# Performance work log

Hardware: AMD Instinct MI355X
Metric: run time of the kernel (lower is better)

## Reference

```python
import jax, jax.numpy as jnp
import numpy as np

NUM_HEADS = 8

def setup_inputs() -> dict:
    key = jax.random.key(0)
    ks = jax.random.split(key, 9)
    b, s, d = 2, 2048, 512
    e = d * NUM_HEADS  # 4096
    sc = 0.02
    return {
        "x": jax.random.normal(ks[0], (b, s, d), jnp.float32),
        "Wq": jax.random.normal(ks[1], (e, d), jnp.float32) * sc,
        "bq": jax.random.normal(ks[2], (e,), jnp.float32) * sc,
        "Wk": jax.random.normal(ks[3], (e, d), jnp.float32) * sc,
        "bk": jax.random.normal(ks[4], (e,), jnp.float32) * sc,
        "Wv": jax.random.normal(ks[5], (e, d), jnp.float32) * sc,
        "bv": jax.random.normal(ks[6], (e,), jnp.float32) * sc,
        "Wo": jax.random.normal(ks[7], (d, e), jnp.float32) * sc,
        "bo": jax.random.normal(ks[8], (d,), jnp.float32) * sc,
    }

def reference(x, Wq, bq, Wk, bk, Wv, bv, Wo, bo):
    b, s, d = x.shape
    h = NUM_HEADS
    hd = d  # head_dim == model_dimension in this module
    # QKV projections: [b, s, h*hd]
    q = (x @ Wq.T + bq).reshape(b, s, h, hd)
    k = (x @ Wk.T + bk).reshape(b, s, h, hd)
    v = (x @ Wv.T + bv).reshape(b, s, h, hd)
    # scores: [b, h, s_q, s_k]
    scores = jnp.einsum("bqhd,bkhd->bhqk", q, k) / jnp.sqrt(jnp.float32(hd))
    attn = jax.nn.softmax(scores, axis=-1)
    ctx = jnp.einsum("bhqk,bkhd->bqhd", attn, v).reshape(b, s, h * hd)
    return ctx @ Wo.T + bo
```

## Files before the change

### kernel.cpp

```cpp
#include <hip/hip_runtime.h>
#include <hip/hip_bf16.h>

typedef __hip_bfloat16 bf16t;
typedef short bf16x8 __attribute__((ext_vector_type(8)));
typedef float f32x4 __attribute__((ext_vector_type(4)));

__device__ __forceinline__ unsigned short f2b(float f) {
    unsigned u;
    __builtin_memcpy(&u, &f, 4);
    unsigned r = (u + 0x7fffu + ((u >> 16) & 1u)) >> 16;
    return (unsigned short)r;
}

__device__ __forceinline__ void gload_lds16(const void* g, void* l) {
    __builtin_amdgcn_global_load_lds(
        (const __attribute__((address_space(1))) void*)g,
        (__attribute__((address_space(3))) void*)l,
        16, 0, 0);
}

__global__ __launch_bounds__(512, 2)
void gemm_qkv(const bf16t* __restrict__ Ag, const bf16t* __restrict__ Bg,
              bf16t* __restrict__ Cg, const float* __restrict__ bias,
              bf16t* __restrict__ VtB, long cOffB)
{
    __shared__ __align__(16) char lds8[131072];

    unsigned gx = gridDim.x, gy = gridDim.y;
    unsigned nwg = gx * gy;
    unsigned wg = blockIdx.y * gx + blockIdx.x;
    if ((nwg & 7u) == 0u) wg = (wg & 7u) * (nwg >> 3) + (wg >> 3);
    const unsigned py = wg / gx;
    const unsigned px = wg - py * gx;
    const int brow = py * 256;
    const int bcol = px * 256;

    const size_t ldab = 1024;
    const size_t ldbb = 1024;
    const char* Agb = (const char*)Ag + (size_t)brow * ldab;
    const char* Bgb = (const char*)Bg + (size_t)bcol * ldbb;

    const int t    = threadIdx.x;
    const int lane = t & 63;
    const int wid  = t >> 6;
    const int wm   = wid >> 2;
    const int wn   = wid & 3;
    const int lr   = lane & 15;
    const int lk   = lane >> 4;

    const int srow = t >> 2;
    const int scg  = (t & 3) ^ ((srow >> 1) & 3);
    const size_t aSrc = (size_t)srow * ldab + (size_t)scg * 16;
    const size_t bSrc = (size_t)srow * ldbb + (size_t)scg * 16;
    const int dst0 = t * 16;
    char* ldsA = lds8;
    char* ldsB = lds8 + 65536;

    const int rchunk = lk ^ ((lr >> 1) & 3);
    const int aByte = (wm * 128 + lr) * 64 + rchunk * 16;
    const int bByte = (wn * 64 + lr) * 64 + rchunk * 16;

    f32x4 acc[8][4];
#pragma unroll
    for (int i = 0; i < 8; ++i)
#pragma unroll
        for (int j = 0; j < 4; ++j)
            acc[i][j] = (f32x4){0.f, 0.f, 0.f, 0.f};

    const int nk = 16;

#define STAGE_A(kt, bufi) do {                                              \
        const char* s_ = Agb + (size_t)(kt) * 64 + aSrc;                    \
        char* d_ = ldsA + (bufi) * 16384 + dst0;                            \
        gload_lds16(s_, d_);                                                \
        gload_lds16(s_ + 128 * ldab, d_ + 8192);                            \
    } while (0)
#define STAGE_B(kt, bufi) do {                                              \
        const char* s_ = Bgb + (size_t)(kt) * 64 + bSrc;                    \
        char* d_ = ldsB + (bufi) * 16384 + dst0;                            \
        gload_lds16(s_, d_);                                                \
        gload_lds16(s_ + 128 * ldbb, d_ + 8192);                            \
    } while (0)

    for (int p = 0; p < 3; ++p) { STAGE_A(p, p & 3); STAGE_B(p, p & 3); }
    asm volatile("s_waitcnt vmcnt(8)" ::: "memory");
    __builtin_amdgcn_s_barrier();

    for (int kt = 0; kt < nk; ++kt) {
        const int buf  = kt & 3;
        const int bufS = (kt + 3) & 3;
        const bool st  = (kt + 3) < nk;
        const char* lA = ldsA + buf * 16384;
        const char* lB = ldsB + buf * 16384;

        bf16x8 af[4], bfv[4];
#pragma unroll
        for (int i = 0; i < 4; ++i) af[i]  = *(const bf16x8*)(lA + aByte + i * 1024);
#pragma unroll
        for (int j = 0; j < 4; ++j) bfv[j] = *(const bf16x8*)(lB + bByte + j * 1024);
        if (st) STAGE_A(kt + 3, bufS);
        __builtin_amdgcn_s_barrier();
        asm volatile("s_waitcnt lgkmcnt(0)" ::: "memory");
        __builtin_amdgcn_s_setprio(1);
#pragma unroll
        for (int i = 0; i < 4; ++i)
#pragma unroll
            for (int j = 0; j < 4; ++j)
                acc[i][j] = __builtin_amdgcn_mfma_f32_16x16x32_bf16(af[i], bfv[j], acc[i][j], 0, 0, 0);
        __builtin_amdgcn_s_setprio(0);
        asm volatile("" ::: "memory");
        __builtin_amdgcn_s_barrier();

        bf16x8 af2[4];
#pragma unroll
        for (int i = 0; i < 4; ++i) af2[i] = *(const bf16x8*)(lA + aByte + (i + 4) * 1024);
        if (st) STAGE_B(kt + 3, bufS);
        if (st)                  asm volatile("s_waitcnt vmcnt(8)" ::: "memory");
        else if (kt + 2 < nk)    asm volatile("s_waitcnt vmcnt(4)" ::: "memory");
        else if (kt + 1 < nk)    asm volatile("s_waitcnt vmcnt(0)" ::: "memory");
        __builtin_amdgcn_s_barrier();
        asm volatile("s_waitcnt lgkmcnt(0)" ::: "memory");
        __builtin_amdgcn_s_setprio(1);
#pragma unroll
        for (int i = 0; i < 4; ++i)
#pragma unroll
            for (int j = 0; j < 4; ++j)
                acc[i + 4][j] = __builtin_amdgcn_mfma_f32_16x16x32_bf16(af2[i], bfv[j], acc[i + 4][j], 0, 0, 0);
        __builtin_amdgcn_s_setprio(0);
        asm volatile("" ::: "memory");
        __builtin_amdgcn_s_barrier();
    }
#undef STAGE_A
#undef STAGE_B

    const int sel = bcol >> 12;
    const int colw0 = bcol & 4095;
    if (sel < 2) {
        __syncthreads();
        unsigned short* lC = (unsigned short*)lds8;
#pragma unroll
        for (int i = 0; i < 8; ++i)
#pragma unroll
            for (int j = 0; j < 4; ++j) {
                int col = wn * 64 + j * 16 + lr;
                float badd = bias[bcol + col];
#pragma unroll
                for (int r = 0; r < 4; ++r) {
                    int row = wm * 128 + i * 16 + lk * 4 + r;
                    lC[row * 256 + col] = f2b(acc[i][j][r] + badd);
                }
            }
        __syncthreads();
        unsigned short* C = (unsigned short*)(Cg + (size_t)sel * cOffB);
#pragma unroll
        for (int p = 0; p < 16; ++p) {
            int c  = p * 512 + t;
            int row = c >> 5;
            int cc  = c & 31;
            bf16x8 v = *(const bf16x8*)(lC + (size_t)c * 8);
            *(bf16x8*)(C + (size_t)(brow + row) * 4096 + colw0 + cc * 8) = v;
        }
    } else {
        unsigned short* C = (unsigned short*)VtB;
#pragma unroll
        for (int i = 0; i < 8; ++i)
#pragma unroll
            for (int j = 0; j < 4; ++j) {
                int col = colw0 + wn * 64 + j * 16 + lr;
                int hh = col >> 9, dd = col & 511;
                float badd = bias[8192 + col];
                int row0 = brow + wm * 128 + i * 16 + lk * 4;
                int bb = row0 >> 11, ss0 = row0 & 2047;
                ushort4 pack;
                pack.x = f2b(acc[i][j][0] + badd);
                pack.y = f2b(acc[i][j][1] + badd);
                pack.z = f2b(acc[i][j][2] + badd);
                pack.w = f2b(acc[i][j][3] + badd);
                size_t addr = ((((size_t)(bb * 8 + hh)) * 512 + dd) << 11) + (size_t)ss0;
                *(ushort4*)(C + addr) = pack;
            }
    }
}

__global__ __launch_bounds__(512, 1)
void attn_fused(const bf16t* __restrict__ Qg, const bf16t* __restrict__ Kg,
                const bf16t* __restrict__ Vtg, bf16t* __restrict__ Esc,
                bf16t* __restrict__ Cg, float scale)
{
    __shared__ __align__(16) char lds[131072];

    unsigned bid = blockIdx.x;
    unsigned swz = (bid & 7u) * 32u + (bid >> 3);
    const int z  = swz >> 4, qt = swz & 15;
    const int zb = z >> 3, zh = z & 7;

    const int t    = threadIdx.x;
    const int lane = t & 63;
    const int wid  = t >> 6;
    const int wm   = wid >> 2;
    const int wn   = wid & 3;
    const int lr   = lane & 15;
    const int lk   = lane >> 4;

    const size_t ldq = 8192;
    const char* Agb = (const char*)Qg + ((size_t)(zb * 2048 + qt * 128) * 4096 + (size_t)zh * 512) * 2;
    const char* Bgb = (const char*)Kg + ((size_t)(zb * 2048) * 4096 + (size_t)zh * 512) * 2;
    unsigned short* Eb = (unsigned short*)(Esc + (size_t)swz * 128 * 2048);

    const int srow = t >> 2;
    const int scg  = (t & 3) ^ ((srow >> 1) & 3);
    const size_t aSrc = (size_t)srow * ldq + (size_t)scg * 16;
    const size_t bSrc = (size_t)srow * ldq + (size_t)scg * 16;
    char* ldsA = lds;
    char* ldsB = lds + 32768;
    const int rchunk = lk ^ ((lr >> 1) & 3);
    const int aByte = (wm * 64 + lr) * 64 + rchunk * 16;
    const int bByte = (wn * 64 + lr) * 64 + rchunk * 16;

    f32x4 acc[4][8];
#pragma unroll
    for (int i = 0; i < 4; ++i)
#pragma unroll
        for (int j = 0; j < 8; ++j)
            acc[i][j] = (f32x4){0.f, 0.f, 0.f, 0.f};
    float rs[4][4];
#pragma unroll
    for (int i = 0; i < 4; ++i)
#pragma unroll
        for (int r = 0; r < 4; ++r)
            rs[i][r] = 0.f;

#define STG_AB(g, bufi) do {                                                \
        gload_lds16(Agb + (size_t)((g) & 15) * 64 + aSrc,                   \
                    ldsA + (bufi) * 8192 + t * 16);                         \
        const char* sb_ = Bgb + (size_t)((g) >> 4) * 256 * ldq              \
                          + (size_t)((g) & 15) * 64 + bSrc;                 \
        char* db_ = ldsB + (bufi) * 16384 + t * 16;                         \
        gload_lds16(sb_, db_);                                              \
        gload_lds16(sb_ + 128 * ldq, db_ + 8192);                           \
    } while (0)

    STG_AB(0, 0); STG_AB(1, 1); STG_AB(2, 2);
    asm volatile("s_waitcnt vmcnt(6)" ::: "memory");
    __builtin_amdgcn_s_barrier();

    for (int g = 0; g < 128; ++g) {
        const int buf = g & 3;
        const char* lA = ldsA + buf * 8192;
        const char* lB = ldsB + buf * 16384;

        bf16x8 af[4], bfv[4];
#pragma unroll
        for (int i = 0; i < 4; ++i) af[i]  = *(const bf16x8*)(lA + aByte + i * 1024);
#pragma unroll
        for (int j = 0; j < 4; ++j) bfv[j] = *(const bf16x8*)(lB + bByte + j * 1024);

        if (g + 3 < 128) {
            STG_AB(g + 3, (g + 3) & 3);
            asm volatile("s_waitcnt vmcnt(6)" ::: "memory");
        } else if (g + 2 < 128) {
            asm volatile("s_waitcnt vmcnt(3)" ::: "memory");
        } else if (g + 1 < 128) {
            asm volatile("s_waitcnt vmcnt(0)" ::: "memory");
        }
        __builtin_amdgcn_s_barrier();
        asm volatile("s_waitcnt lgkmcnt(0)" ::: "memory");
        __builtin_amdgcn_s_setprio(1);
#pragma unroll
        for (int i = 0; i < 4; ++i)
#pragma unroll
            for (int j = 0; j < 4; ++j)
                acc[i][j] = __builtin_amdgcn_mfma_f32_16x16x32_bf16(af[i], bfv[j], acc[i][j], 0, 0, 0);
        __builtin_amdgcn_s_setprio(0);
        asm volatile("" ::: "memory");
        __builtin_amdgcn_s_barrier();

        if ((g & 15) == 15) {
            const int nt = g >> 4;
#pragma unroll
            for (int i = 0; i < 4; ++i)
#pragma unroll
                for (int j = 0; j < 4; ++j)
#pragma unroll
                    for (int r = 0; r < 4; ++r)
                        acc[i][j][r] = __expf(acc[i][j][r] * scale);
#pragma unroll
            for (int i = 0; i < 4; ++i)
#pragma unroll
                for (int r = 0; r < 4; ++r)
                    rs[i][r] += acc[i][0][r] + acc[i][1][r] + acc[i][2][r] + acc[i][3][r];

            unsigned short* epi = (unsigned short*)(lds + 98304);
#pragma unroll
            for (int m = 0; m < 2; ++m) {
                if (wm == m) {
#pragma unroll
                    for (int i = 0; i < 4; ++i)
#pragma unroll
                        for (int j = 0; j < 4; ++j) {
                            int col = wn * 64 + j * 16 + lr;
#pragma unroll
                            for (int r = 0; r < 4; ++r)
                                epi[(i * 16 + lk * 4 + r) * 256 + col] = f2b(acc[i][j][r]);
                        }
                }
                asm volatile("s_waitcnt lgkmcnt(0)" ::: "memory");
                __builtin_amdgcn_s_barrier();
#pragma unroll
                for (int p = 0; p < 4; ++p) {
                    int c  = p * 512 + t;
                    int row = c >> 5;
                    int cc  = c & 31;
                    bf16x8 v = *(const bf16x8*)(epi + (size_t)c * 8);
                    *(bf16x8*)(Eb + (size_t)(m * 64 + row) * 2048 + nt * 256 + cc * 8) = v;
                }
                asm volatile("s_waitcnt lgkmcnt(0)" ::: "memory");
                __builtin_amdgcn_s_barrier();
            }
#pragma unroll
            for (int i = 0; i < 4; ++i)
#pragma unroll
                for (int j = 0; j < 4; ++j)
                    acc[i][j] = (f32x4){0.f, 0.f, 0.f, 0.f};
        }
    }
#undef STG_AB

    asm volatile("s_waitcnt vmcnt(0) lgkmcnt(0)" ::: "memory");
    __builtin_amdgcn_s_barrier();

#pragma unroll
    for (int i = 0; i < 4; ++i)
#pragma unroll
        for (int r = 0; r < 4; ++r) {
            float v = rs[i][r];
            v += __shfl_xor(v, 1);
            v += __shfl_xor(v, 2);
            v += __shfl_xor(v, 4);
            v += __shfl_xor(v, 8);
            rs[i][r] = v;
        }
    float* tbl = (float*)(lds + 98304);
    if (lr == 0) {
#pragma unroll
        for (int i = 0; i < 4; ++i)
#pragma unroll
            for (int r = 0; r < 4; ++r)
                tbl[(wm * 64 + i * 16 + lk * 4 + r) * 4 + wn] = rs[i][r];
    }
    asm volatile("s_waitcnt lgkmcnt(0)" ::: "memory");
    __builtin_amdgcn_s_barrier();
    float inv_[4][4];
#pragma unroll
    for (int i = 0; i < 4; ++i)
#pragma unroll
        for (int r = 0; r < 4; ++r) {
            int row = wm * 64 + i * 16 + lk * 4 + r;
            float4 v4 = *(const float4*)(tbl + row * 4);
            inv_[i][r] = 1.0f / (v4.x + v4.y + v4.z + v4.w);
        }
    asm volatile("s_waitcnt lgkmcnt(0)" ::: "memory");
    __builtin_amdgcn_s_barrier();

    const char* A2 = (const char*)Eb;
    const char* B2 = (const char*)Vtg + (size_t)z * 512 * 2048 * 2;
    char* ldsA2 = lds;
    char* ldsB2 = lds + 24576;
    const size_t a2Src = (size_t)srow * 4096 + (size_t)scg * 16;
    const size_t b2Src = (size_t)srow * 4096 + (size_t)scg * 16;
    const int bByte2 = (wn * 128 + lr) * 64 + rchunk * 16;

#pragma unroll
    for (int i = 0; i < 4; ++i)
#pragma unroll
        for (int j = 0; j < 8; ++j)
            acc[i][j] = (f32x4){0.f, 0.f, 0.f, 0.f};

#define STG_PV(kt, bufi) do {                                               \
        gload_lds16(A2 + (size_t)(kt) * 64 + a2Src,                         \
                    ldsA2 + (bufi) * 8192 + t * 16);                        \
        const char* sb_ = B2 + (size_t)(kt) * 64 + b2Src;                   \
        char* db_ = ldsB2 + (bufi) * 32768 + t * 16;                        \
        gload_lds16(sb_,              db_);                                 \
        gload_lds16(sb_ + 128 * 4096, db_ + 8192);                          \
        gload_lds16(sb_ + 256 * 4096, db_ + 16384);                         \
        gload_lds16(sb_ + 384 * 4096, db_ + 24576);                         \
    } while (0)

    STG_PV(0, 0);
    STG_PV(1, 1);
    asm volatile("s_waitcnt vmcnt(5)" ::: "memory");
    __builtin_amdgcn_s_barrier();

    int bufR = 0, bufS = 2;
    for (int kt = 0; kt < 64; ++kt) {
        const char* lA = ldsA2 + bufR * 8192;
        const char* lB = ldsB2 + bufR * 32768;

        bf16x8 af[4], bfv[8];
#pragma unroll
        for (int i = 0; i < 4; ++i) af[i]  = *(const bf16x8*)(lA + aByte + i * 1024);
#pragma unroll
        for (int j = 0; j < 8; ++j) bfv[j] = *(const bf16x8*)(lB + bByte2 + j * 1024);

        if (kt + 2 < 64) {
            STG_PV(kt + 2, bufS);
            asm volatile("s_waitcnt vmcnt(5)" ::: "memory");
        } else if (kt + 1 < 64) {
            asm volatile("s_waitcnt vmcnt(0)" ::: "memory");
        }
        __builtin_amdgcn_s_barrier();
        asm volatile("s_waitcnt lgkmcnt(0)" ::: "memory");
        __builtin_amdgcn_s_setprio(1);
#pragma unroll
        for (int i = 0; i < 4; ++i)
#pragma unroll
            for (int j = 0; j < 8; ++j)
                acc[i][j] = __builtin_amdgcn_mfma_f32_16x16x32_bf16(af[i], bfv[j], acc[i][j], 0, 0, 0);
        __builtin_amdgcn_s_setprio(0);
        asm volatile("" ::: "memory");
        __builtin_amdgcn_s_barrier();

        bufR = (bufR == 2) ? 0 : bufR + 1;
        bufS = (bufS == 2) ? 0 : bufS + 1;
    }
#undef STG_PV

    unsigned short* lC = (unsigned short*)lds;
    unsigned short* C = (unsigned short*)Cg + (size_t)zb * 2048 * 4096 + (size_t)zh * 512;
#pragma unroll
    for (int m = 0; m < 2; ++m) {
        __syncthreads();
        if (wm == m) {
#pragma unroll
            for (int i = 0; i < 4; ++i)
#pragma unroll
                for (int j = 0; j < 8; ++j) {
                    int col = wn * 128 + j * 16 + lr;
#pragma unroll
                    for (int r = 0; r < 4; ++r) {
                        int row = i * 16 + lk * 4 + r;
                        lC[row * 512 + col] = f2b(acc[i][j][r] * inv_[i][r]);
                    }
                }
        }
        __syncthreads();
#pragma unroll
        for (int p = 0; p < 8; ++p) {
            int c  = p * 512 + t;
            int row = c >> 6;
            int cc  = c & 63;
            bf16x8 v = *(const bf16x8*)(lC + (size_t)c * 8);
            *(bf16x8*)(C + (size_t)(qt * 128 + m * 64 + row) * 4096 + cc * 8) = v;
        }
    }
}

__global__ __launch_bounds__(256, 3)
void gemm_of32(const bf16t* __restrict__ Ag, const bf16t* __restrict__ Bg,
               float* __restrict__ Cg, const float* __restrict__ bias,
               int K, int lda, int ldb, int ldc)
{
    __shared__ __align__(16) char lds[49152];

    unsigned gx = gridDim.x, gy = gridDim.y;
    unsigned nwg = gx * gy;
    unsigned wg = blockIdx.y * gx + blockIdx.x;
    if ((nwg & 7u) == 0u) wg = (wg & 7u) * (nwg >> 3) + (wg >> 3);
    const unsigned py = wg / gx;
    const unsigned px = wg - py * gx;
    const int brow = py * 128;
    const int bcol = px * 64;

    const int t    = threadIdx.x;
    const int lane = t & 63;
    const int wid  = t >> 6;
    const int wr   = wid >> 1, wc = wid & 1;
    const int lr   = lane & 15;
    const int lk   = lane >> 4;

    const size_t ldab = (size_t)lda * 2;
    const size_t ldbb = (size_t)ldb * 2;
    const char* Agb = (const char*)Ag + (size_t)brow * ldab;
    const char* Bgb = (const char*)Bg + (size_t)bcol * ldbb;

    const int srow = t >> 2;
    const int scg  = (t & 3) ^ ((srow >> 1) & 3);
    const size_t aSrc = (size_t)srow * ldab + (size_t)scg * 16;
    const size_t bSrc = (size_t)srow * ldbb + (size_t)scg * 16;
    char* ldsA = lds;
    char* ldsB = lds + 32768;

    const int rchunk = lk ^ ((lr >> 1) & 3);
    const int aByte = (wr * 64 + lr) * 64 + rchunk * 16;
    const int bByte = (wc * 32 + lr) * 64 + rchunk * 16;

    f32x4 acc[4][2];
#pragma unroll
    for (int i = 0; i < 4; ++i)
#pragma unroll
        for (int j = 0; j < 2; ++j)
            acc[i][j] = (f32x4){0.f, 0.f, 0.f, 0.f};

    const int nk = K >> 5;

#define STAGE_O(kt, bufi) do {                                              \
        const char* sa_ = Agb + (size_t)(kt) * 64 + aSrc;                   \
        gload_lds16(sa_,             ldsA + (bufi) * 8192 + t * 16);        \
        gload_lds16(sa_ + 64 * ldab, ldsA + (bufi) * 8192 + 4096 + t * 16); \
        gload_lds16(Bgb + (size_t)(kt) * 64 + bSrc,                         \
                    ldsB + (bufi) * 4096 + t * 16);                         \
    } while (0)

    for (int p = 0; p < 3; ++p) STAGE_O(p, p);
    asm volatile("s_waitcnt vmcnt(6)" ::: "memory");
    __builtin_amdgcn_s_barrier();

    for (int kt = 0; kt < nk; ++kt) {
        const int buf  = kt & 3;
        const bool st  = (kt + 3) < nk;
        const char* lA = ldsA + buf * 8192;
        const char* lB = ldsB + buf * 4096;

        bf16x8 af[4], bfv[2];
#pragma unroll
        for (int i = 0; i < 4; ++i) af[i]  = *(const bf16x8*)(lA + aByte + i * 1024);
#pragma unroll
        for (int j = 0; j < 2; ++j) bfv[j] = *(const bf16x8*)(lB + bByte + j * 1024);
        if (st) STAGE_O(kt + 3, (kt + 3) & 3);
        if (st)                  asm volatile("s_waitcnt vmcnt(6)" ::: "memory");
        else if (kt + 2 < nk)    asm volatile("s_waitcnt vmcnt(3)" ::: "memory");
        else if (kt + 1 < nk)    asm volatile("s_waitcnt vmcnt(0)" ::: "memory");
        __builtin_amdgcn_s_barrier();
        asm volatile("s_waitcnt lgkmcnt(0)" ::: "memory");
        __builtin_amdgcn_s_setprio(1);
#pragma unroll
        for (int i = 0; i < 4; ++i)
#pragma unroll
            for (int j = 0; j < 2; ++j)
                acc[i][j] = __builtin_amdgcn_mfma_f32_16x16x32_bf16(af[i], bfv[j], acc[i][j], 0, 0, 0);
        __builtin_amdgcn_s_setprio(0);
        asm volatile("" ::: "memory");
        __builtin_amdgcn_s_barrier();
    }
#undef STAGE_O

    const int orow = brow + wr * 64;
    const int ocol = bcol + wc * 32;
#pragma unroll
    for (int i = 0; i < 4; ++i)
#pragma unroll
        for (int j = 0; j < 2; ++j) {
            int col = ocol + j * 16 + lr;
            float badd = bias[col];
#pragma unroll
            for (int r = 0; r < 4; ++r) {
                int row = orow + i * 16 + lk * 4 + r;
                Cg[(size_t)row * ldc + col] = acc[i][j][r] + badd;
            }
        }
}

__global__ __launch_bounds__(256)
void cvt6(const float* __restrict__ s0, const float* __restrict__ s1,
          const float* __restrict__ s2, const float* __restrict__ s3,
          const float* __restrict__ s4,
          bf16t* __restrict__ d0, bf16t* __restrict__ d1,
          bf16t* __restrict__ d2, bf16t* __restrict__ d3,
          bf16t* __restrict__ d4,
          const float* __restrict__ bq, const float* __restrict__ bk,
          const float* __restrict__ bv, float* __restrict__ bqkv)
{
    int i = blockIdx.x * 256 + threadIdx.x;
    if (blockIdx.y == 5) {
        if (i < 3072) {
            int e = i * 4;
            const float* src = (e < 4096) ? (bq + e) : (e < 8192) ? (bk + e - 4096) : (bv + e - 8192);
            float4 f = *(const float4*)src;
            *(float4*)(bqkv + e) = f;
        }
        return;
    }
    const float* s;
    bf16t* d;
    switch (blockIdx.y) {
        case 0: s = s0; d = d0; break;
        case 1: s = s1; d = d1; break;
        case 2: s = s2; d = d2; break;
        case 3: s = s3; d = d3; break;
        default: s = s4; d = d4; break;
    }
    float4 f = ((const float4*)s)[i];
    ushort4 o;
    o.x = f2b(f.x); o.y = f2b(f.y); o.z = f2b(f.z); o.w = f2b(f.w);
    ((ushort4*)d)[i] = o;
}

extern "C" void kernel_launch(void* const* d_in, const int* in_sizes, int n_in,
                              void* d_out, int out_size, void* d_ws, size_t ws_size,
                              hipStream_t stream)
{
    const float* x  = (const float*)d_in[0];
    const float* Wq = (const float*)d_in[1];
    const float* bq = (const float*)d_in[2];
    const float* Wk = (const float*)d_in[3];
    const float* bk = (const float*)d_in[4];
    const float* Wv = (const float*)d_in[5];
    const float* bv = (const float*)d_in[6];
    const float* Wo = (const float*)d_in[7];
    const float* bo = (const float*)d_in[8];

    const int Sn = 2048, Dn = 512, En = 4096;
    const int Mn = 4096;
    const float scl = 0.044194173824159216f;

    bf16t* base = (bf16t*)d_ws;
    size_t off = 0;
    bf16t* Qb  = base + off; off += (size_t)Mn * En;
    bf16t* Kb  = base + off; off += (size_t)Mn * En;
    bf16t* Vt  = base + off; off += (size_t)Mn * En;
    bf16t* Xb  = base + off; off += (size_t)Mn * Dn;
    bf16t* Wc  = base + off; off += (size_t)3 * En * Dn;
    bf16t* Wob = base + off; off += (size_t)Dn * En;
    float* Pbias = (float*)(base + off); off += 12288;
    bf16t* Sb  = base + off;

    cvt6<<<dim3(2048, 6, 1), 256, 0, stream>>>(
        x, Wq, Wk, Wv, Wo,
        Xb, Wc, Wc + (size_t)En * Dn, Wc + (size_t)2 * En * Dn, Wob,
        bq, bk, bv, Pbias);

    gemm_qkv<<<dim3(3 * En / 256, Mn / 256, 1), 512, 0, stream>>>(
        Xb, Wc, Qb, Pbias, Vt, (long)Mn * En);

    attn_fused<<<256, 512, 0, stream>>>(Qb, Kb, Vt, Sb, Qb, scl);

    gemm_of32<<<dim3(Dn / 64, Mn / 128, 1), 256, 0, stream>>>(
        Qb, Wob, (float*)d_out, bo, En, En, En, Dn);
}
```

Baseline: 293.7 us.

## Fuse P·V into the QK loop, keeping exp scores in LDS

The attention kernel used to write the full 128x2048 exp-score tile to a global scratch buffer and then run a separate P·V GEMM that read it back. Now, after each 256-key block of QK^T, it writes the exp scores as bf16 into a swizzled LDS region and immediately multiplies them by the matching V^T slab into a persistent accumulator. This removes the global round trip for the scores and the scratch buffer, at the cost of 160KB of LDS, more accumulator registers live at once, and extra barriers per key block. There is still no running max, so it relies on unshifted exp as before.

Measured after the change: 471.7 us. +60.6%, slower.

```diff
diff --git a/kernel.cpp b/kernel.cpp
--- a/kernel.cpp
+++ b/kernel.cpp
@@ -183,11 +183,11 @@
 }
 
 __global__ __launch_bounds__(512, 1)
-void attn_fused(const bf16t* __restrict__ Qg, const bf16t* __restrict__ Kg,
-                const bf16t* __restrict__ Vtg, bf16t* __restrict__ Esc,
-                bf16t* __restrict__ Cg, float scale)
+void attn_flash(const bf16t* __restrict__ Qg, const bf16t* __restrict__ Kg,
+                const bf16t* __restrict__ Vtg, bf16t* __restrict__ Cg,
+                float scale)
 {
-    __shared__ __align__(16) char lds[131072];
+    __shared__ __align__(16) char lds[163840];
 
     unsigned bid = blockIdx.x;
     unsigned swz = (bid & 7u) * 32u + (bid >> 3);
@@ -204,25 +204,29 @@
 
     const size_t ldq = 8192;
     const char* Agb = (const char*)Qg + ((size_t)(zb * 2048 + qt * 128) * 4096 + (size_t)zh * 512) * 2;
-    const char* Bgb = (const char*)Kg + ((size_t)(zb * 2048) * 4096 + (size_t)zh * 512) * 2;
-    unsigned short* Eb = (unsigned short*)(Esc + (size_t)swz * 128 * 2048);
+    const char* Kgb = (const char*)Kg + ((size_t)(zb * 2048) * 4096 + (size_t)zh * 512) * 2;
+    const char* Vgb = (const char*)Vtg + (size_t)z * 512 * 2048 * 2;
 
     const int srow = t >> 2;
     const int scg  = (t & 3) ^ ((srow >> 1) & 3);
-    const size_t aSrc = (size_t)srow * ldq + (size_t)scg * 16;
-    const size_t bSrc = (size_t)srow * ldq + (size_t)scg * 16;
-    char* ldsA = lds;
-    char* ldsB = lds + 32768;
+    const size_t qSrc = (size_t)srow * ldq + (size_t)scg * 16;
+    const size_t vSrc = (size_t)srow * 4096 + (size_t)scg * 16;
+    char* ldsQ = lds;
+    char* ldsK = lds + 32768;
+    char* ldsV = lds;
+    char* Elds = lds + 98304;
+
     const int rchunk = lk ^ ((lr >> 1) & 3);
     const int aByte = (wm * 64 + lr) * 64 + rchunk * 16;
     const int bByte = (wn * 64 + lr) * 64 + rchunk * 16;
-
-    f32x4 acc[4][8];
+    const int vByte = (wn * 128 + lr) * 64 + rchunk * 16;
+
+    f32x4 accC[4][8];
 #pragma unroll
     for (int i = 0; i < 4; ++i)
 #pragma unroll
         for (int j = 0; j < 8; ++j)
-            acc[i][j] = (f32x4){0.f, 0.f, 0.f, 0.f};
+            accC[i][j] = (f32x4){0.f, 0.f, 0.f, 0.f};
     float rs[4][4];
 #pragma unroll
     for (int i = 0; i < 4; ++i)
@@ -230,104 +234,130 @@
         for (int r = 0; r < 4; ++r)
             rs[i][r] = 0.f;
 
-#define STG_AB(g, bufi) do {                                                \
-        gload_lds16(Agb + (size_t)((g) & 15) * 64 + aSrc,                   \
-                    ldsA + (bufi) * 8192 + t * 16);                         \
-        const char* sb_ = Bgb + (size_t)((g) >> 4) * 256 * ldq              \
-                          + (size_t)((g) & 15) * 64 + bSrc;                 \
-        char* db_ = ldsB + (bufi) * 16384 + t * 16;                         \
-        gload_lds16(sb_, db_);                                              \
-        gload_lds16(sb_ + 128 * ldq, db_ + 8192);                           \
+#define STG_QK(nt, ks, bufi) do {                                           \
+        gload_lds16(Agb + (size_t)(ks) * 64 + qSrc,                         \
+                    ldsQ + (bufi) * 8192 + t * 16);                         \
+        const char* sk_ = Kgb + (size_t)(nt) * 256 * ldq                    \
+                          + (size_t)(ks) * 64 + qSrc;                       \
+        char* dk_ = ldsK + (bufi) * 16384 + t * 16;                         \
+        gload_lds16(sk_, dk_);                                              \
+        gload_lds16(sk_ + 128 * ldq, dk_ + 8192);                           \
     } while (0)
-
-    STG_AB(0, 0); STG_AB(1, 1); STG_AB(2, 2);
-    asm volatile("s_waitcnt vmcnt(6)" ::: "memory");
-    __builtin_amdgcn_s_barrier();
-
-    for (int g = 0; g < 128; ++g) {
-        const int buf = g & 3;
-        const char* lA = ldsA + buf * 8192;
-        const char* lB = ldsB + buf * 16384;
-
-        bf16x8 af[4], bfv[4];
-#pragma unroll
-        for (int i = 0; i < 4; ++i) af[i]  = *(const bf16x8*)(lA + aByte + i * 1024);
-#pragma unroll
-        for (int j = 0; j < 4; ++j) bfv[j] = *(const bf16x8*)(lB + bByte + j * 1024);
-
-        if (g + 3 < 128) {
-            STG_AB(g + 3, (g + 3) & 3);
-            asm volatile("s_waitcnt vmcnt(6)" ::: "memory");
-        } else if (g + 2 < 128) {
-            asm volatile("s_waitcnt vmcnt(3)" ::: "memory");
-        } else if (g + 1 < 128) {
-            asm volatile("s_waitcnt vmcnt(0)" ::: "memory");
-        }
-        __builtin_amdgcn_s_barrier();
+#define STG_V(nt, c, bufi) do {                                             \
+        const char* sv_ = Vgb + (size_t)(nt) * 512 + (size_t)(c) * 64 + vSrc;\
+        char* dv_ = ldsV + (bufi) * 32768 + t * 16;                         \
+        gload_lds16(sv_,              dv_);                                 \
+        gload_lds16(sv_ + 128 * 4096, dv_ + 8192);                          \
+        gload_lds16(sv_ + 256 * 4096, dv_ + 16384);                         \
+        gload_lds16(sv_ + 384 * 4096, dv_ + 24576);                         \
+    } while (0)
+
+    for (int nt = 0; nt < 8; ++nt) {
+        f32x4 accA[4][4];
+#pragma unroll
+        for (int i = 0; i < 4; ++i)
+#pragma unroll
+            for (int j = 0; j < 4; ++j)
+                accA[i][j] = (f32x4){0.f, 0.f, 0.f, 0.f};
+
+        STG_QK(nt, 0, 0); STG_QK(nt, 1, 1); STG_QK(nt, 2, 2);
+        asm volatile("s_waitcnt vmcnt(6)" ::: "memory");
+        __builtin_amdgcn_s_barrier();
+
+        for (int ks = 0; ks < 16; ++ks) {
+            const int buf = ks & 3;
+            const char* lA = ldsQ + buf * 8192;
+            const char* lB = ldsK + buf * 16384;
+
+            bf16x8 af[4], bfv[4];
+#pragma unroll
+            for (int i = 0; i < 4; ++i) af[i]  = *(const bf16x8*)(lA + aByte + i * 1024);
+#pragma unroll
+            for (int j = 0; j < 4; ++j) bfv[j] = *(const bf16x8*)(lB + bByte + j * 1024);
+
+            if (ks + 3 < 16) {
+                STG_QK(nt, ks + 3, (ks + 3) & 3);
+                asm volatile("s_waitcnt vmcnt(6)" ::: "memory");
+            } else if (ks + 2 < 16) {
+                asm volatile("s_waitcnt vmcnt(3)" ::: "memory");
+            } else if (ks + 1 < 16) {
+                asm volatile("s_waitcnt vmcnt(0)" ::: "memory");
+            }
+            __builtin_amdgcn_s_barrier();
+            asm volatile("s_waitcnt lgkmcnt(0)" ::: "memory");
+            __builtin_amdgcn_s_setprio(1);
+#pragma unroll
+            for (int i = 0; i < 4; ++i)
+#pragma unroll
+                for (int j = 0; j < 4; ++j)
+                    accA[i][j] = __builtin_amdgcn_mfma_f32_16x16x32_bf16(af[i], bfv[j], accA[i][j], 0, 0, 0);
+            __builtin_amdgcn_s_setprio(0);
+            asm volatile("" ::: "memory");
+            __builtin_amdgcn_s_barrier();
+        }
+
+        unsigned short* Ew = (unsigned short*)Elds;
+#pragma unroll
+        for (int i = 0; i < 4; ++i)
+#pragma unroll
+            for (int j = 0; j < 4; ++j) {
+                int col = wn * 64 + j * 16 + lr;
+#pragma unroll
+                for (int r = 0; r < 4; ++r) {
+                    float e = __expf(accA[i][j][r] * scale);
+                    accA[i][j][r] = e;
+                    int row = wm * 64 + i * 16 + lk * 4 + r;
+                    int slot = (col >> 3) ^ (row & 7);
+                    Ew[row * 256 + slot * 8 + (col & 7)] = f2b(e);
+                }
+            }
+#pragma unroll
+        for (int i = 0; i < 4; ++i)
+#pragma unroll
+            for (int r = 0; r < 4; ++r)
+                rs[i][r] += accA[i][0][r] + accA[i][1][r] + accA[i][2][r] + accA[i][3][r];
         asm volatile("s_waitcnt lgkmcnt(0)" ::: "memory");
-        __builtin_amdgcn_s_setprio(1);
-#pragma unroll
-        for (int i = 0; i < 4; ++i)
-#pragma unroll
-            for (int j = 0; j < 4; ++j)
-                acc[i][j] = __builtin_amdgcn_mfma_f32_16x16x32_bf16(af[i], bfv[j], acc[i][j], 0, 0, 0);
-        __builtin_amdgcn_s_setprio(0);
-        asm volatile("" ::: "memory");
-        __builtin_amdgcn_s_barrier();
-
-        if ((g & 15) == 15) {
-            const int nt = g >> 4;
+        __builtin_amdgcn_s_barrier();
+
+        STG_V(nt, 0, 0); STG_V(nt, 1, 1);
+        asm volatile("s_waitcnt vmcnt(4)" ::: "memory");
+        __builtin_amdgcn_s_barrier();
+
+        for (int c = 0; c < 8; ++c) {
+            const int bufv = c % 3;
+            const char* lV = ldsV + bufv * 32768;
+
+            bf16x8 afE[4], bfvV[8];
+#pragma unroll
+            for (int i = 0; i < 4; ++i) {
+                int row = wm * 64 + i * 16 + lr;
+                int slot = (c * 4 + lk) ^ (lr & 7);
+                afE[i] = *(const bf16x8*)(Elds + (size_t)row * 512 + (size_t)slot * 16);
+            }
+#pragma unroll
+            for (int j = 0; j < 8; ++j) bfvV[j] = *(const bf16x8*)(lV + vByte + j * 1024);
+
+            if (c + 2 < 8) {
+                STG_V(nt, c + 2, (c + 2) % 3);
+                asm volatile("s_waitcnt vmcnt(4)" ::: "memory");
+            } else if (c + 1 < 8) {
+                asm volatile("s_waitcnt vmcnt(0)" ::: "memory");
+            }
+            __builtin_amdgcn_s_barrier();
+            asm volatile("s_waitcnt lgkmcnt(0)" ::: "memory");
+            __builtin_amdgcn_s_setprio(1);
 #pragma unroll
             for (int i = 0; i < 4; ++i)
 #pragma unroll
-                for (int j = 0; j < 4; ++j)
-#pragma unroll
-                    for (int r = 0; r < 4; ++r)
-                        acc[i][j][r] = __expf(acc[i][j][r] * scale);
-#pragma unroll
-            for (int i = 0; i < 4; ++i)
-#pragma unroll
-                for (int r = 0; r < 4; ++r)
-                    rs[i][r] += acc[i][0][r] + acc[i][1][r] + acc[i][2][r] + acc[i][3][r];
-
-            unsigned short* epi = (unsigned short*)(lds + 98304);
-#pragma unroll
-            for (int m = 0; m < 2; ++m) {
-                if (wm == m) {
-#pragma unroll
-                    for (int i = 0; i < 4; ++i)
-#pragma unroll
-                        for (int j = 0; j < 4; ++j) {
-                            int col = wn * 64 + j * 16 + lr;
-#pragma unroll
-                            for (int r = 0; r < 4; ++r)
-                                epi[(i * 16 + lk * 4 + r) * 256 + col] = f2b(acc[i][j][r]);
-                        }
-                }
-                asm volatile("s_waitcnt lgkmcnt(0)" ::: "memory");
-                __builtin_amdgcn_s_barrier();
-#pragma unroll
-                for (int p = 0; p < 4; ++p) {
-                    int c  = p * 512 + t;
-                    int row = c >> 5;
-                    int cc  = c & 31;
-                    bf16x8 v = *(const bf16x8*)(epi + (size_t)c * 8);
-                    *(bf16x8*)(Eb + (size_t)(m * 64 + row) * 2048 + nt * 256 + cc * 8) = v;
-                }
-                asm volatile("s_waitcnt lgkmcnt(0)" ::: "memory");
-                __builtin_amdgcn_s_barrier();
-            }
-#pragma unroll
-            for (int i = 0; i < 4; ++i)
-#pragma unroll
-                for (int j = 0; j < 4; ++j)
-                    acc[i][j] = (f32x4){0.f, 0.f, 0.f, 0.f};
-        }
-    }
-#undef STG_AB
-
-    asm volatile("s_waitcnt vmcnt(0) lgkmcnt(0)" ::: "memory");
-    __builtin_amdgcn_s_barrier();
+                for (int j = 0; j < 8; ++j)
+                    accC[i][j] = __builtin_amdgcn_mfma_f32_16x16x32_bf16(afE[i], bfvV[j], accC[i][j], 0, 0, 0);
+            __builtin_amdgcn_s_setprio(0);
+            asm volatile("" ::: "memory");
+            __builtin_amdgcn_s_barrier();
+        }
+    }
+#undef STG_QK
+#undef STG_V
 
 #pragma unroll
     for (int i = 0; i < 4; ++i)
@@ -340,7 +370,8 @@
             v += __shfl_xor(v, 8);
             rs[i][r] = v;
         }
-    float* tbl = (float*)(lds + 98304);
+    __syncthreads();
+    float* tbl = (float*)Elds;
     if (lr == 0) {
 #pragma unroll
         for (int i = 0; i < 4; ++i)
@@ -348,8 +379,7 @@
             for (int r = 0; r < 4; ++r)
                 tbl[(wm * 64 + i * 16 + lk * 4 + r) * 4 + wn] = rs[i][r];
     }
-    asm volatile("s_waitcnt lgkmcnt(0)" ::: "memory");
-    __builtin_amdgcn_s_barrier();
+    __syncthreads();
     float inv_[4][4];
 #pragma unroll
     for (int i = 0; i < 4; ++i)
@@ -359,72 +389,6 @@
             float4 v4 = *(const float4*)(tbl + row * 4);
             inv_[i][r] = 1.0f / (v4.x + v4.y + v4.z + v4.w);
         }
-    asm volatile("s_waitcnt lgkmcnt(0)" ::: "memory");
-    __builtin_amdgcn_s_barrier();
-
-    const char* A2 = (const char*)Eb;
-    const char* B2 = (const char*)Vtg + (size_t)z * 512 * 2048 * 2;
-    char* ldsA2 = lds;
-    char* ldsB2 = lds + 24576;
-    const size_t a2Src = (size_t)srow * 4096 + (size_t)scg * 16;
-    const size_t b2Src = (size_t)srow * 4096 + (size_t)scg * 16;
-    const int bByte2 = (wn * 128 + lr) * 64 + rchunk * 16;
-
-#pragma unroll
-    for (int i = 0; i < 4; ++i)
-#pragma unroll
-        for (int j = 0; j < 8; ++j)
-            acc[i][j] = (f32x4){0.f, 0.f, 0.f, 0.f};
-
-#define STG_PV(kt, bufi) do {                                               \
-        gload_lds16(A2 + (size_t)(kt) * 64 + a2Src,                         \
-                    ldsA2 + (bufi) * 8192 + t * 16);                        \
-        const char* sb_ = B2 + (size_t)(kt) * 64 + b2Src;                   \
-        char* db_ = ldsB2 + (bufi) * 32768 + t * 16;                        \
-        gload_lds16(sb_,              db_);                                 \
-        gload_lds16(sb_ + 128 * 4096, db_ + 8192);                          \
-        gload_lds16(sb_ + 256 * 4096, db_ + 16384);                         \
-        gload_lds16(sb_ + 384 * 4096, db_ + 24576);                         \
-    } while (0)
-
-    STG_PV(0, 0);
-    STG_PV(1, 1);
-    asm volatile("s_waitcnt vmcnt(5)" ::: "memory");
-    __builtin_amdgcn_s_barrier();
-
-    int bufR = 0, bufS = 2;
-    for (int kt = 0; kt < 64; ++kt) {
-        const char* lA = ldsA2 + bufR * 8192;
-        const char* lB = ldsB2 + bufR * 32768;
-
-        bf16x8 af[4], bfv[8];
-#pragma unroll
-        for (int i = 0; i < 4; ++i) af[i]  = *(const bf16x8*)(lA + aByte + i * 1024);
-#pragma unroll
-        for (int j = 0; j < 8; ++j) bfv[j] = *(const bf16x8*)(lB + bByte2 + j * 1024);
-
-        if (kt + 2 < 64) {
-            STG_PV(kt + 2, bufS);
-            asm volatile("s_waitcnt vmcnt(5)" ::: "memory");
-        } else if (kt + 1 < 64) {
-            asm volatile("s_waitcnt vmcnt(0)" ::: "memory");
-        }
-        __builtin_amdgcn_s_barrier();
-        asm volatile("s_waitcnt lgkmcnt(0)" ::: "memory");
-        __builtin_amdgcn_s_setprio(1);
-#pragma unroll
-        for (int i = 0; i < 4; ++i)
-#pragma unroll
-            for (int j = 0; j < 8; ++j)
-                acc[i][j] = __builtin_amdgcn_mfma_f32_16x16x32_bf16(af[i], bfv[j], acc[i][j], 0, 0, 0);
-        __builtin_amdgcn_s_setprio(0);
-        asm volatile("" ::: "memory");
-        __builtin_amdgcn_s_barrier();
-
-        bufR = (bufR == 2) ? 0 : bufR + 1;
-        bufS = (bufS == 2) ? 0 : bufS + 1;
-    }
-#undef STG_PV
 
     unsigned short* lC = (unsigned short*)lds;
     unsigned short* C = (unsigned short*)Cg + (size_t)zb * 2048 * 4096 + (size_t)zh * 512;
@@ -440,7 +404,7 @@
 #pragma unroll
                     for (int r = 0; r < 4; ++r) {
                         int row = i * 16 + lk * 4 + r;
-                        lC[row * 512 + col] = f2b(acc[i][j][r] * inv_[i][r]);
+                        lC[row * 512 + col] = f2b(accC[i][j][r] * inv_[i][r]);
                     }
                 }
         }
@@ -610,7 +574,7 @@
     const float* Wo = (const float*)d_in[7];
     const float* bo = (const float*)d_in[8];
 
-    const int Sn = 2048, Dn = 512, En = 4096;
+    const int Dn = 512, En = 4096;
     const int Mn = 4096;
     const float scl = 0.044194173824159216f;
 
@@ -623,7 +587,6 @@
     bf16t* Wc  = base + off; off += (size_t)3 * En * Dn;
     bf16t* Wob = base + off; off += (size_t)Dn * En;
     float* Pbias = (float*)(base + off); off += 12288;
-    bf16t* Sb  = base + off;
 
     cvt6<<<dim3(2048, 6, 1), 256, 0, stream>>>(
         x, Wq, Wk, Wv, Wo,
@@ -633,7 +596,7 @@
     gemm_qkv<<<dim3(3 * En / 256, Mn / 256, 1), 512, 0, stream>>>(
         Xb, Wc, Qb, Pbias, Vt, (long)Mn * En);
 
-    attn_fused<<<256, 512, 0, stream>>>(Qb, Kb, Vt, Sb, Qb, scl);
+    attn_flash<<<256, 512, 0, stream>>>(Qb, Kb, Vt, Qb, scl);
 
     gemm_of32<<<dim3(Dn / 64, Mn / 128, 1), 256, 0, stream>>>(
         Qb, Wob, (float*)d_out, bo, En, En, En, Dn);
```
